# Optimization experiments

Hardware: AMD Instinct MI355X
Metric: run time of the kernel (lower is better)

## Reference

```python
import jax, jax.numpy as jnp
import numpy as np

B, N = 32, 64
ATTR, STATE, REL, GDIM = 4, 8, 4, 32
NF = 128

def _ln(x, w, b, eps=1e-5):
    mu = jnp.mean(x, axis=-1, keepdims=True)
    var = jnp.mean((x - mu) ** 2, axis=-1, keepdims=True)
    return (x - mu) * jax.lax.rsqrt(var + eps) * w + b

def setup_inputs() -> dict:
    key = jax.random.key(0)
    ks = iter(jax.random.split(key, 32))
    d = {}
    d['attrs'] = jax.random.normal(next(ks), (B, N, ATTR), jnp.float32)
    d['states'] = jax.random.normal(next(ks), (B, N, STATE), jnp.float32)
    d['actions'] = jnp.zeros((B, N, 4), jnp.float32)  # action=False, unused
    d['rel_attrs'] = jax.random.normal(next(ks), (B, N, N, REL), jnp.float32)
    def w(shape):
        return jax.random.normal(next(ks), shape, jnp.float32) * 0.05
    d['oe_w0'] = w((NF, ATTR + STATE)); d['oe_b0'] = jnp.zeros((NF,), jnp.float32)
    d['oe_w1'] = w((NF, NF));            d['oe_b1'] = jnp.zeros((NF,), jnp.float32)
    d['re_w0'] = w((NF, STATE + REL + 2 * ATTR)); d['re_b0'] = jnp.zeros((NF,), jnp.float32)
    d['re_w1'] = w((NF, NF));            d['re_b1'] = jnp.zeros((NF,), jnp.float32)
    d['rp_w'] = w((NF, NF + 2 * NF));    d['rp_b'] = jnp.zeros((NF,), jnp.float32)
    d['rp_lnw'] = jnp.ones((NF,), jnp.float32); d['rp_lnb'] = jnp.zeros((NF,), jnp.float32)
    d['pp_w'] = w((NF, 2 * NF));         d['pp_b'] = jnp.zeros((NF,), jnp.float32)
    d['pp_lnw'] = jnp.ones((NF,), jnp.float32); d['pp_lnb'] = jnp.zeros((NF,), jnp.float32)
    d['pr_w0'] = w((NF, NF));            d['pr_b0'] = jnp.zeros((NF,), jnp.float32)
    d['pr_w1'] = w((GDIM, NF));          d['pr_b1'] = jnp.zeros((GDIM,), jnp.float32)
    d['pstep'] = 2
    return d

def reference(attrs, states, actions, rel_attrs,
              oe_w0, oe_b0, oe_w1, oe_b1,
              re_w0, re_b0, re_w1, re_b1,
              rp_w, rp_b, rp_lnw, rp_lnb,
              pp_w, pp_b, pp_lnw, pp_lnb,
              pr_w0, pr_b0, pr_w1, pr_b1, pstep):
    lin = lambda x, w, b: jnp.einsum('...i,oi->...o', x, w) + b
    # ---- encode nodes: [B,N,attr+state] -> [B,N,NF] (action=False) ----
    obj_in = jnp.concatenate([attrs, states], axis=2)
    obj_encode = jax.nn.relu(lin(jax.nn.relu(lin(obj_in, oe_w0, oe_b0)), oe_w1, oe_b1))
    # ---- encode edges over dense N x N pairs ----
    rel_states = states[:, :, None, :] - states[:, None, :, :]        # B,N,N,state
    recv_attr = jnp.broadcast_to(attrs[:, :, None, :], (attrs.shape[0], attrs.shape[1], attrs.shape[1], attrs.shape[2]))
    send_attr = jnp.broadcast_to(attrs[:, None, :, :], recv_attr.shape)
    rel_in = jnp.concatenate([rel_attrs, rel_states, recv_attr, send_attr], axis=3)
    rel_encode = jax.nn.relu(lin(jax.nn.relu(lin(rel_in, re_w0, re_b0)), re_w1, re_b1))  # B,N,N,NF
    # ---- propagation steps ----
    for _ in range(pstep):
        sh = rel_encode.shape[:3] + (obj_encode.shape[-1],)
        recv = jnp.broadcast_to(obj_encode[:, :, None, :], sh)
        send = jnp.broadcast_to(obj_encode[:, None, :, :], sh)
        rel_effect = jax.nn.relu(_ln(lin(jnp.concatenate([rel_encode, recv, send], axis=3), rp_w, rp_b), rp_lnw, rp_lnb))
        rel_agg = rel_effect.sum(axis=2)                               # B,N,NF
        obj_encode = jax.nn.relu(_ln(lin(jnp.concatenate([obj_encode, rel_agg], axis=2), pp_w, pp_b), pp_lnw, pp_lnb))
    # ---- predict + tanh (state_encoder has tanh=True) ----
    out = lin(jax.nn.relu(lin(obj_encode, pr_w0, pr_b0)), pr_w1, pr_b1)
    return jnp.tanh(out)
```

## Files before the change

### kernel.cpp

```cpp
#include <hip/hip_runtime.h>
#include <hip/hip_bf16.h>


#define ROWS 2048
typedef unsigned short u16;
typedef unsigned int u32;
typedef __attribute__((ext_vector_type(8))) short bf16x8;
typedef __attribute__((ext_vector_type(4))) float f32x4;

__device__ __forceinline__ float bsu(u16 u) { return __uint_as_float(((u32)u) << 16); }
__device__ __forceinline__ u16 f2b(float f) {
    u32 u = __float_as_uint(f);
    u32 r = (u + 0x7fffu + ((u >> 16) & 1u)) >> 16;
    return (u16)r;
}
__device__ __forceinline__ u32 pk2(float a, float b) {
    __hip_bfloat162 h = __float22bfloat162_rn(float2{a, b});
    union { __hip_bfloat162 h; u32 u; } c; c.h = h; return c.u;
}
__device__ __forceinline__ bf16x8 ldcvt8(const float* __restrict__ p) {
    float4 a = *(const float4*)p;
    float4 b = *(const float4*)(p + 4);
    union { u32 u[4]; bf16x8 v; } x;
    x.u[0] = pk2(a.x, a.y); x.u[1] = pk2(a.z, a.w);
    x.u[2] = pk2(b.x, b.y); x.u[3] = pk2(b.z, b.w);
    return x.v;
}

__global__ __launch_bounds__(256)
void k_node(const float* __restrict__ attrs, const float* __restrict__ states,
            const float* __restrict__ oe_w0, const float* __restrict__ oe_b0,
            const float* __restrict__ oe_w1, const float* __restrict__ oe_b1,
            const float* __restrict__ re_w0, const float* __restrict__ re_b0,
            const float* __restrict__ rp_w,  const float* __restrict__ rp_b,
            const float* __restrict__ re_w1, const float* __restrict__ pp_w,
            const float* __restrict__ pr_w0, const float* __restrict__ pr_w1,
            u16* __restrict__ re_w1b, u16* __restrict__ web, u16* __restrict__ pp_wb,
            u16* __restrict__ wrecvb, u16* __restrict__ wsendb,
            u16* __restrict__ pr_w0b, u16* __restrict__ pr_w1b, u16* __restrict__ wsumb,
            u16* __restrict__ objb, float* __restrict__ nr, float* __restrict__ ns,
            float* __restrict__ recvT, float* __restrict__ sendT,
            float* __restrict__ recvS0, float* __restrict__ sendS0)
{
    const int r0 = blockIdx.x * 16;
    const int t = threadIdx.x;
    __shared__ float xs[16][12];
    __shared__ float w0s[1536];
    __shared__ float rw0s[2560];
    __shared__ __align__(16) u16 hb[16 * 136];
    __shared__ __align__(16) u16 ob[16 * 136];

    {
        int gid = blockIdx.x * 256 + t;
        for (int i = gid; i < 118784; i += 32768) {
            int idx = i;
            if (idx < 16384) { re_w1b[idx] = f2b(re_w1[idx]); continue; }
            idx -= 16384;
            if (idx < 16384) { web[idx] = f2b(rp_w[(idx >> 7) * 384 + (idx & 127)]); continue; }
            idx -= 16384;
            if (idx < 32768) { pp_wb[idx] = f2b(pp_w[idx]); continue; }
            idx -= 32768;
            if (idx < 16384) { wrecvb[idx] = f2b(rp_w[(idx >> 7) * 384 + 128 + (idx & 127)]); continue; }
            idx -= 16384;
            if (idx < 16384) { wsendb[idx] = f2b(rp_w[(idx >> 7) * 384 + 256 + (idx & 127)]); continue; }
            idx -= 16384;
            if (idx < 16384) { pr_w0b[idx] = f2b(pr_w0[idx]); continue; }
            idx -= 16384;
            pr_w1b[idx] = f2b(pr_w1[idx]);
        }
    }
    if (blockIdx.x == 0 && t < 128) {
        float s = 0.f;
        for (int o = 0; o < 128; o++) s += bsu(f2b(rp_w[o * 384 + t]));
        wsumb[t] = f2b(s);
    }

    if (t < 192) { int row = t / 12, c = t - row * 12;
        xs[row][c] = (c < 4) ? attrs[(r0 + row) * 4 + c] : states[(r0 + row) * 8 + (c - 4)]; }
    for (int i = t; i < 1536; i += 256) w0s[i] = oe_w0[i];
    for (int i = t; i < 2560; i += 256) rw0s[i] = re_w0[i];
    __syncthreads();

    for (int e = t; e < 2048; e += 256) {
        int row = e >> 7, o = e & 127;
        float h = oe_b0[o];
#pragma unroll
        for (int k = 0; k < 12; k++) h += w0s[o * 12 + k] * xs[row][k];
        hb[row * 136 + o] = f2b(fmaxf(h, 0.f));
        float s0 = 0.f, a0 = 0.f, a1 = 0.f;
#pragma unroll
        for (int k = 0; k < 8; k++) s0 += rw0s[o * 20 + 4 + k] * xs[row][4 + k];
#pragma unroll
        for (int k = 0; k < 4; k++) {
            a0 += rw0s[o * 20 + 12 + k] * xs[row][k];
            a1 += rw0s[o * 20 + 16 + k] * xs[row][k];
        }
        nr[(r0 + row) * 128 + o] = s0 + a0 + re_b0[o];
        ns[(r0 + row) * 128 + o] = a1 - s0;
    }
    __syncthreads();

    const int wave = t >> 6, lane = t & 63, tx = lane & 15, quad = lane >> 4;

    bf16x8 afr[4];
#pragma unroll
    for (int kk = 0; kk < 4; kk++) afr[kk] = *(const bf16x8*)&hb[tx * 136 + kk * 32 + quad * 8];
    f32x4 acc[2]; acc[0] = (f32x4){0.f,0.f,0.f,0.f}; acc[1] = acc[0];
#pragma unroll
    for (int ot = 0; ot < 2; ot++) {
        int o = (wave * 2 + ot) * 16 + tx;
#pragma unroll
        for (int kk = 0; kk < 4; kk++) {
            bf16x8 bfr = ldcvt8(&oe_w1[o * 128 + kk * 32 + quad * 8]);
            acc[ot] = __builtin_amdgcn_mfma_f32_16x16x32_bf16(afr[kk], bfr, acc[ot], 0, 0, 0);
        }
    }
#pragma unroll
    for (int ot = 0; ot < 2; ot++) {
        int o = (wave * 2 + ot) * 16 + tx;
        float bia = oe_b1[o];
#pragma unroll
        for (int r = 0; r < 4; r++)
            ob[(quad * 4 + r) * 136 + o] = f2b(fmaxf(acc[ot][r] + bia, 0.f));
    }
    __syncthreads();
    { int m = t >> 4, c = t & 15;
      *(uint4*)&objb[(r0 + m) * 128 + c * 8] = *(const uint4*)&ob[m * 136 + c * 8]; }

#pragma unroll
    for (int kk = 0; kk < 4; kk++) afr[kk] = *(const bf16x8*)&ob[tx * 136 + kk * 32 + quad * 8];
    f32x4 ar[2], an[2];
    ar[0] = (f32x4){0.f,0.f,0.f,0.f}; ar[1] = ar[0]; an[0] = ar[0]; an[1] = ar[0];
#pragma unroll
    for (int ot = 0; ot < 2; ot++) {
        int o = (wave * 2 + ot) * 16 + tx;
#pragma unroll
        for (int kk = 0; kk < 4; kk++) {
            bf16x8 br = ldcvt8(&rp_w[o * 384 + 128 + kk * 32 + quad * 8]);
            ar[ot] = __builtin_amdgcn_mfma_f32_16x16x32_bf16(afr[kk], br, ar[ot], 0, 0, 0);
            bf16x8 bs = ldcvt8(&rp_w[o * 384 + 256 + kk * 32 + quad * 8]);
            an[ot] = __builtin_amdgcn_mfma_f32_16x16x32_bf16(afr[kk], bs, an[ot], 0, 0, 0);
        }
    }
    float rbv[2] = { rp_b[(wave * 2 + 0) * 16 + tx], rp_b[(wave * 2 + 1) * 16 + tx] };
#pragma unroll
    for (int ot = 0; ot < 2; ot++) {
        int o = (wave * 2 + ot) * 16 + tx;
#pragma unroll
        for (int r = 0; r < 4; r++) {
            recvT[(r0 + quad * 4 + r) * 128 + o] = ar[ot][r] + rbv[ot];
            sendT[(r0 + quad * 4 + r) * 128 + o] = an[ot][r];
        }
    }
    __syncthreads();
    float* fr  = (float*)hb;
    float* fs2 = (float*)ob;
#pragma unroll
    for (int r = 0; r < 4; r++) {
        int row = quad * 4 + r;
        fr[row * 68 + wave * 16 + tx]  = (ar[0][r] + rbv[0]) + (ar[1][r] + rbv[1]);
        fs2[row * 68 + wave * 16 + tx] = an[0][r] + an[1][r];
    }
    __syncthreads();
    if (t < 32) {
        int p = t >> 4, row = t & 15;
        const float* src = p ? fs2 : fr;
        float s = 0.f;
#pragma unroll
        for (int k = 0; k < 64; k++) s += src[row * 68 + k];
        (p ? sendS0 : recvS0)[r0 + row] = s;
    }
}

__global__ __launch_bounds__(256)
void k_edge_fused(const float* __restrict__ rel_attrs,
                  const float* __restrict__ re_w0, const u16* __restrict__ re_w1b,
                  const u16* __restrict__ web, const u16* __restrict__ wsumb,
                  const float* __restrict__ re_b1,
                  const float* __restrict__ rp_lnw, const float* __restrict__ rp_lnb,
                  const float* __restrict__ nr, const float* __restrict__ ns,
                  const float* __restrict__ recvT, const float* __restrict__ sendT,
                  const float* __restrict__ recvS0, const float* __restrict__ sendS0,
                  u16* __restrict__ Ebuf, float* __restrict__ rowsumE,
                  u16* __restrict__ aggb)
{
    const int blkg = blockIdx.x;
    const int b = blkg >> 6;
    const int t = threadIdx.x;
    __shared__ __align__(16) u16 hsb[64 * 144];
    __shared__ float lnws[128], lnbs[128];
    __shared__ float redQ[256];

    if (t < 128) { lnws[t] = rp_lnw[t]; lnbs[t] = rp_lnb[t]; }

    {
        const int o0 = (t & 15) * 8;
        const int jb = t >> 4;
        float4 nr0 = *(const float4*)&nr[blkg * 128 + o0];
        float4 nr1 = *(const float4*)&nr[blkg * 128 + o0 + 4];
        float4 wreg[8];
#pragma unroll
        for (int k = 0; k < 8; k++) wreg[k] = *(const float4*)&re_w0[(o0 + k) * 20];
#pragma unroll
        for (int it = 0; it < 4; it++) {
            int j = jb + it * 16;
            float4 ra = *(const float4*)&rel_attrs[((size_t)blkg * 64 + j) * 4];
            const float* nsp = &ns[(b * 64 + j) * 128 + o0];
            float4 na = *(const float4*)nsp;
            float4 nb = *(const float4*)(nsp + 4);
            float v[8];
            v[0] = nr0.x + na.x; v[1] = nr0.y + na.y; v[2] = nr0.z + na.z; v[3] = nr0.w + na.w;
            v[4] = nr1.x + nb.x; v[5] = nr1.y + nb.y; v[6] = nr1.z + nb.z; v[7] = nr1.w + nb.w;
#pragma unroll
            for (int k = 0; k < 8; k++) {
                v[k] += wreg[k].x * ra.x + wreg[k].y * ra.y + wreg[k].z * ra.z + wreg[k].w * ra.w;
                v[k] = fmaxf(v[k], 0.f);
            }
            union { u32 u[4]; uint4 q; } p;
            p.u[0] = pk2(v[0], v[1]); p.u[1] = pk2(v[2], v[3]);
            p.u[2] = pk2(v[4], v[5]); p.u[3] = pk2(v[6], v[7]);
            *(uint4*)&hsb[j * 144 + o0] = p.q;
        }
    }

    const int w = t >> 6, lane = t & 63, tx = lane & 15, quad = lane >> 4;
    const int ob = w * 32;

    bf16x8 b1[2][4];
#pragma unroll
    for (int ot = 0; ot < 2; ot++)
#pragma unroll
        for (int kk = 0; kk < 4; kk++)
            b1[ot][kk] = *(const bf16x8*)&re_w1b[(ob + ot * 16 + tx) * 128 + kk * 32 + quad * 8];
    __syncthreads();

    f32x4 acc[4][2];
#pragma unroll
    for (int jt = 0; jt < 4; jt++) { acc[jt][0] = (f32x4){0.f,0.f,0.f,0.f}; acc[jt][1] = acc[jt][0]; }
#pragma unroll
    for (int jt = 0; jt < 4; jt++) {
        bf16x8 afr[4];
#pragma unroll
        for (int kk = 0; kk < 4; kk++)
            afr[kk] = *(const bf16x8*)&hsb[(jt * 16 + tx) * 144 + kk * 32 + quad * 8];
#pragma unroll
        for (int ot = 0; ot < 2; ot++)
#pragma unroll
            for (int kk = 0; kk < 4; kk++)
                acc[jt][ot] = __builtin_amdgcn_mfma_f32_16x16x32_bf16(afr[kk], b1[ot][kk], acc[jt][ot], 0, 0, 0);
    }
    __syncthreads();

    {
        float bia0 = re_b1[ob + tx], bia1 = re_b1[ob + 16 + tx];
#pragma unroll
        for (int jt = 0; jt < 4; jt++)
#pragma unroll
            for (int r = 0; r < 4; r++) {
                int j = jt * 16 + quad * 4 + r;
                hsb[j * 144 + ob + tx]      = f2b(fmaxf(acc[jt][0][r] + bia0, 0.f));
                hsb[j * 144 + ob + 16 + tx] = f2b(fmaxf(acc[jt][1][r] + bia1, 0.f));
            }
    }
    bf16x8 b2[2][4];
#pragma unroll
    for (int ot = 0; ot < 2; ot++)
#pragma unroll
        for (int kk = 0; kk < 4; kk++)
            b2[ot][kk] = *(const bf16x8*)&web[(ob + ot * 16 + tx) * 128 + kk * 32 + quad * 8];
    bf16x8 bws[4];
#pragma unroll
    for (int kk = 0; kk < 4; kk++)
        bws[kk] = *(const bf16x8*)&wsumb[kk * 32 + quad * 8];
    __syncthreads();

    f32x4 acc2[4][2], acc_ws[4];
#pragma unroll
    for (int jt = 0; jt < 4; jt++) {
        acc2[jt][0] = (f32x4){0.f,0.f,0.f,0.f}; acc2[jt][1] = acc2[jt][0];
        acc_ws[jt] = acc2[jt][0];
    }
#pragma unroll
    for (int jt = 0; jt < 4; jt++) {
        bf16x8 afr[4];
#pragma unroll
        for (int kk = 0; kk < 4; kk++)
            afr[kk] = *(const bf16x8*)&hsb[(jt * 16 + tx) * 144 + kk * 32 + quad * 8];
#pragma unroll
        for (int ot = 0; ot < 2; ot++)
#pragma unroll
            for (int kk = 0; kk < 4; kk++)
                acc2[jt][ot] = __builtin_amdgcn_mfma_f32_16x16x32_bf16(afr[kk], b2[ot][kk], acc2[jt][ot], 0, 0, 0);
#pragma unroll
        for (int kk = 0; kk < 4; kk++)
            acc_ws[jt] = __builtin_amdgcn_mfma_f32_16x16x32_bf16(afr[kk], bws[kk], acc_ws[jt], 0, 0, 0);
    }

#pragma unroll
    for (int jt = 0; jt < 4; jt++)
#pragma unroll
        for (int ot = 0; ot < 2; ot++) {
            uint2 ev;
            ev.x = pk2(acc2[jt][ot][0], acc2[jt][ot][1]);
            ev.y = pk2(acc2[jt][ot][2], acc2[jt][ot][3]);
            *(uint2*)(Ebuf + ((size_t)((blkg * 4 + jt) * 8 + (2 * w + ot)) * 64 + lane) * 4) = ev;
        }
    if (w == 0 && tx == 0) {
#pragma unroll
        for (int jt = 0; jt < 4; jt++)
            *(f32x4*)&rowsumE[(size_t)blkg * 64 + jt * 16 + quad * 4] = acc_ws[jt];
    }

    {
        float rv0 = recvT[blkg * 128 + ob + tx];
        float rv1 = recvT[blkg * 128 + ob + 16 + tx];
#pragma unroll
        for (int jt = 0; jt < 4; jt++)
#pragma unroll
            for (int r = 0; r < 4; r++) {
                int j = b * 64 + jt * 16 + quad * 4 + r;
                acc2[jt][0][r] += rv0 + sendT[j * 128 + ob + tx];
                acc2[jt][1][r] += rv1 + sendT[j * 128 + ob + 16 + tx];
            }
    }

#pragma unroll
    for (int jt = 0; jt < 4; jt++) {
        float q4[4];
#pragma unroll
        for (int r = 0; r < 4; r++) {
            float a0 = acc2[jt][0][r], a1 = acc2[jt][1][r];
            q4[r] = a0 * a0 + a1 * a1;
        }
#pragma unroll
        for (int m = 1; m < 16; m <<= 1)
#pragma unroll
            for (int r = 0; r < 4; r++) q4[r] += __shfl_xor(q4[r], m, 64);
        if (tx == 0)
#pragma unroll
            for (int r = 0; r < 4; r++) redQ[w * 64 + jt * 16 + quad * 4 + r] = q4[r];
    }
    __syncthreads();

    {
        float recvSi = recvS0[blkg];
        float lw0 = lnws[ob + tx], lb0 = lnbs[ob + tx];
        float lw1 = lnws[ob + 16 + tx], lb1 = lnbs[ob + 16 + tx];
        float ag0 = 0.f, ag1 = 0.f;
#pragma unroll
        for (int jt = 0; jt < 4; jt++) {
            f32x4 ssf = *(const f32x4*)&sendS0[b * 64 + jt * 16 + quad * 4];
#pragma unroll
            for (int r = 0; r < 4; r++) {
                int row = jt * 16 + quad * 4 + r;
                float qq = redQ[row] + redQ[64 + row] + redQ[128 + row] + redQ[192 + row];
                float mu = (acc_ws[jt][r] + recvSi + ssf[r]) * (1.f / 128.f);
                float rsd = rsqrtf(qq * (1.f / 128.f) - mu * mu + 1e-5f);
                float z0 = (acc2[jt][0][r] - mu) * rsd * lw0 + lb0;
                float z1 = (acc2[jt][1][r] - mu) * rsd * lw1 + lb1;
                ag0 += fmaxf(z0, 0.f);
                ag1 += fmaxf(z1, 0.f);
            }
        }
        ag0 += __shfl_xor(ag0, 16, 64); ag0 += __shfl_xor(ag0, 32, 64);
        ag1 += __shfl_xor(ag1, 16, 64); ag1 += __shfl_xor(ag1, 32, 64);
        if (quad == 0) {
            aggb[blkg * 128 + ob + tx]      = f2b(ag0);
            aggb[blkg * 128 + ob + 16 + tx] = f2b(ag1);
        }
    }
}

__global__ __launch_bounds__(256)
void k_prop_edge2(const u16* __restrict__ Ebuf, const float* __restrict__ rowsumE,
                  const float* __restrict__ rp_lnw, const float* __restrict__ rp_lnb,
                  const float* __restrict__ recvT, const float* __restrict__ sendT,
                  const float* __restrict__ recvS1, const float* __restrict__ sendS1,
                  u16* __restrict__ aggb)
{
    const int blk = blockIdx.x;
    const int b = blk >> 6;
    const int t = threadIdx.x;
    __shared__ float scr[16 * 132];
    __shared__ float lnws[128], lnbs[128];
    if (t < 128) { lnws[t] = rp_lnw[t]; lnbs[t] = rp_lnb[t]; }
    __syncthreads();

    const int wave = t >> 6, lane = t & 63, tx = lane & 15, quad = lane >> 4;
    const int tid = blk * 4 + wave;
    const int jrow = wave * 16 + quad * 4;

    float y[8][4];
#pragma unroll
    for (int oo = 0; oo < 8; oo++) {
        uint2 ev = *(const uint2*)(Ebuf + ((size_t)(tid * 8 + oo) * 64 + lane) * 4);
        const int o = oo * 16 + tx;
        float rv = recvT[blk * 128 + o];
        float e0 = bsu((u16)(ev.x & 0xffff)), e1 = bsu((u16)(ev.x >> 16));
        float e2 = bsu((u16)(ev.y & 0xffff)), e3 = bsu((u16)(ev.y >> 16));
        y[oo][0] = e0 + rv + sendT[(b * 64 + jrow + 0) * 128 + o];
        y[oo][1] = e1 + rv + sendT[(b * 64 + jrow + 1) * 128 + o];
        y[oo][2] = e2 + rv + sendT[(b * 64 + jrow + 2) * 128 + o];
        y[oo][3] = e3 + rv + sendT[(b * 64 + jrow + 3) * 128 + o];
    }
    float q[4];
#pragma unroll
    for (int r = 0; r < 4; r++) {
        q[r] = 0.f;
#pragma unroll
        for (int oo = 0; oo < 8; oo++) q[r] += y[oo][r] * y[oo][r];
    }
#pragma unroll
    for (int m = 1; m < 16; m <<= 1)
#pragma unroll
        for (int r = 0; r < 4; r++) q[r] += __shfl_xor(q[r], m, 64);

    float recvSi = recvS1[blk];
    f32x4 rse = *(const f32x4*)&rowsumE[(size_t)blk * 64 + jrow];
    f32x4 ssf = *(const f32x4*)&sendS1[b * 64 + jrow];
    float mu[4], rs[4];
#pragma unroll
    for (int r = 0; r < 4; r++) {
        mu[r] = (rse[r] + recvSi + ssf[r]) * (1.f / 128.f);
        rs[r] = rsqrtf(q[r] * (1.f / 128.f) - mu[r] * mu[r] + 1e-5f);
    }
    float pa[8];
#pragma unroll
    for (int oo = 0; oo < 8; oo++) {
        const int o = oo * 16 + tx;
        float lw = lnws[o], lb = lnbs[o];
        float p = 0.f;
#pragma unroll
        for (int r = 0; r < 4; r++) {
            float z = (y[oo][r] - mu[r]) * rs[r] * lw + lb;
            p += fmaxf(z, 0.f);
        }
        pa[oo] = p;
    }
    const int grp = wave * 4 + quad;
#pragma unroll
    for (int oo = 0; oo < 8; oo++) scr[grp * 132 + oo * 16 + tx] = pa[oo];
    __syncthreads();
    if (t < 128) {
        float sum = 0.f;
#pragma unroll
        for (int gg = 0; gg < 16; gg++) sum += scr[gg * 132 + t];
        aggb[blk * 128 + t] = f2b(sum);
    }
}

__global__ __launch_bounds__(256)
void k_pn0(const u16* __restrict__ aggb,
           const u16* __restrict__ pp_wb, const float* __restrict__ pp_b,
           const float* __restrict__ pp_lnw, const float* __restrict__ pp_lnb,
           const u16* __restrict__ wrecvb, const u16* __restrict__ wsendb,
           const float* __restrict__ rp_b,
           u16* __restrict__ objb, float* __restrict__ recvT, float* __restrict__ sendT,
           float* __restrict__ recvS1, float* __restrict__ sendS1)
{
    const int r0 = blockIdx.x * 16;
    const int t = threadIdx.x;
    __shared__ __align__(16) u16 ab[16 * 264];
    __shared__ __align__(16) u16 ob[16 * 136];
    __shared__ float redS[64], redQ[64];

    for (int i = t; i < 512; i += 256) {
        int m = i >> 5, c = i & 31;
        uint4 v = (c < 16) ? *(const uint4*)&objb[(r0 + m) * 128 + (c & 15) * 8]
                           : *(const uint4*)&aggb[(r0 + m) * 128 + (c - 16) * 8];
        *(uint4*)&ab[m * 264 + c * 8] = v;
    }
    __syncthreads();

    const int wave = t >> 6, lane = t & 63, tx = lane & 15, quad = lane >> 4;
    bf16x8 afr[8];
#pragma unroll
    for (int kk = 0; kk < 8; kk++) afr[kk] = *(const bf16x8*)&ab[tx * 264 + kk * 32 + quad * 8];
    f32x4 acc[2]; acc[0] = (f32x4){0.f,0.f,0.f,0.f}; acc[1] = acc[0];
#pragma unroll
    for (int ot = 0; ot < 2; ot++) {
        int o = (wave * 2 + ot) * 16 + tx;
#pragma unroll
        for (int kk = 0; kk < 8; kk++) {
            bf16x8 bfr = *(const bf16x8*)&pp_wb[o * 256 + kk * 32 + quad * 8];
            acc[ot] = __builtin_amdgcn_mfma_f32_16x16x32_bf16(afr[kk], bfr, acc[ot], 0, 0, 0);
        }
    }
#pragma unroll
    for (int ot = 0; ot < 2; ot++) {
        float bia = pp_b[(wave * 2 + ot) * 16 + tx];
#pragma unroll
        for (int r = 0; r < 4; r++) acc[ot][r] += bia;
    }

    float s[4], q[4];
#pragma unroll
    for (int r = 0; r < 4; r++) {
        s[r] = acc[0][r] + acc[1][r];
        q[r] = acc[0][r] * acc[0][r] + acc[1][r] * acc[1][r];
    }
#pragma unroll
    for (int m = 1; m < 16; m <<= 1) {
#pragma unroll
        for (int r = 0; r < 4; r++) {
            s[r] += __shfl_xor(s[r], m, 64);
            q[r] += __shfl_xor(q[r], m, 64);
        }
    }
    if (tx == 0) {
#pragma unroll
        for (int r = 0; r < 4; r++) {
            redS[wave * 16 + quad * 4 + r] = s[r];
            redQ[wave * 16 + quad * 4 + r] = q[r];
        }
    }
    __syncthreads();
    float mu[4], rs[4];
#pragma unroll
    for (int r = 0; r < 4; r++) {
        int m = quad * 4 + r;
        float ss = redS[m] + redS[16 + m] + redS[32 + m] + redS[48 + m];
        float qq = redQ[m] + redQ[16 + m] + redQ[32 + m] + redQ[48 + m];
        mu[r] = ss * (1.f / 128.f);
        rs[r] = rsqrtf(qq * (1.f / 128.f) - mu[r] * mu[r] + 1e-5f);
    }
#pragma unroll
    for (int ot = 0; ot < 2; ot++) {
        int o = (wave * 2 + ot) * 16 + tx;
        float lw = pp_lnw[o], lb = pp_lnb[o];
#pragma unroll
        for (int r = 0; r < 4; r++) {
            float z = (acc[ot][r] - mu[r]) * rs[r] * lw + lb;
            ob[(quad * 4 + r) * 136 + o] = f2b(fmaxf(z, 0.f));
        }
    }
    __syncthreads();
    { int m = t >> 4, c = t & 15;
      *(uint4*)&objb[(r0 + m) * 128 + c * 8] = *(const uint4*)&ob[m * 136 + c * 8]; }

    bf16x8 af2[4];
#pragma unroll
    for (int kk = 0; kk < 4; kk++) af2[kk] = *(const bf16x8*)&ob[tx * 136 + kk * 32 + quad * 8];
    f32x4 ar[2], an[2];
    ar[0] = (f32x4){0.f,0.f,0.f,0.f}; ar[1] = ar[0]; an[0] = ar[0]; an[1] = ar[0];
#pragma unroll
    for (int ot = 0; ot < 2; ot++) {
        int o = (wave * 2 + ot) * 16 + tx;
#pragma unroll
        for (int kk = 0; kk < 4; kk++) {
            bf16x8 br = *(const bf16x8*)&wrecvb[o * 128 + kk * 32 + quad * 8];
            ar[ot] = __builtin_amdgcn_mfma_f32_16x16x32_bf16(af2[kk], br, ar[ot], 0, 0, 0);
            bf16x8 bs = *(const bf16x8*)&wsendb[o * 128 + kk * 32 + quad * 8];
            an[ot] = __builtin_amdgcn_mfma_f32_16x16x32_bf16(af2[kk], bs, an[ot], 0, 0, 0);
        }
    }
    float rbv[2] = { rp_b[(wave * 2 + 0) * 16 + tx], rp_b[(wave * 2 + 1) * 16 + tx] };
#pragma unroll
    for (int ot = 0; ot < 2; ot++) {
        int o = (wave * 2 + ot) * 16 + tx;
#pragma unroll
        for (int r = 0; r < 4; r++) {
            recvT[(r0 + quad * 4 + r) * 128 + o] = ar[ot][r] + rbv[ot];
            sendT[(r0 + quad * 4 + r) * 128 + o] = an[ot][r];
        }
    }
    __syncthreads();
    float* fr  = (float*)ab;
    float* fs2 = ((float*)ab) + 1056;
#pragma unroll
    for (int r = 0; r < 4; r++) {
        int row = quad * 4 + r;
        fr[row * 66 + wave * 16 + tx]  = (ar[0][r] + rbv[0]) + (ar[1][r] + rbv[1]);
        fs2[row * 66 + wave * 16 + tx] = an[0][r] + an[1][r];
    }
    __syncthreads();
    if (t < 32) {
        int p = t >> 4, row = t & 15;
        const float* src = p ? fs2 : fr;
        float s2 = 0.f;
#pragma unroll
        for (int k = 0; k < 64; k++) s2 += src[row * 66 + k];
        (p ? sendS1 : recvS1)[r0 + row] = s2;
    }
}

__global__ __launch_bounds__(256)
void k_pn1pred(const u16* __restrict__ aggb,
               const u16* __restrict__ pp_wb, const float* __restrict__ pp_b,
               const float* __restrict__ pp_lnw, const float* __restrict__ pp_lnb,
               const u16* __restrict__ objb,
               const u16* __restrict__ pr_w0b, const float* __restrict__ pr_b0,
               const u16* __restrict__ pr_w1b, const float* __restrict__ pr_b1,
               float* __restrict__ out)
{
    const int r0 = blockIdx.x * 16;
    const int t = threadIdx.x;
    __shared__ __align__(16) u16 ab[16 * 264];
    __shared__ __align__(16) u16 ob[16 * 136];
    __shared__ __align__(16) u16 hb2[16 * 136];
    __shared__ float redS[64], redQ[64];

    for (int i = t; i < 512; i += 256) {
        int m = i >> 5, c = i & 31;
        uint4 v = (c < 16) ? *(const uint4*)&objb[(r0 + m) * 128 + (c & 15) * 8]
                           : *(const uint4*)&aggb[(r0 + m) * 128 + (c - 16) * 8];
        *(uint4*)&ab[m * 264 + c * 8] = v;
    }
    __syncthreads();

    const int wave = t >> 6, lane = t & 63, tx = lane & 15, quad = lane >> 4;
    bf16x8 afr[8];
#pragma unroll
    for (int kk = 0; kk < 8; kk++) afr[kk] = *(const bf16x8*)&ab[tx * 264 + kk * 32 + quad * 8];
    f32x4 acc[2]; acc[0] = (f32x4){0.f,0.f,0.f,0.f}; acc[1] = acc[0];
#pragma unroll
    for (int ot = 0; ot < 2; ot++) {
        int o = (wave * 2 + ot) * 16 + tx;
#pragma unroll
        for (int kk = 0; kk < 8; kk++) {
            bf16x8 bfr = *(const bf16x8*)&pp_wb[o * 256 + kk * 32 + quad * 8];
            acc[ot] = __builtin_amdgcn_mfma_f32_16x16x32_bf16(afr[kk], bfr, acc[ot], 0, 0, 0);
        }
    }
#pragma unroll
    for (int ot = 0; ot < 2; ot++) {
        float bia = pp_b[(wave * 2 + ot) * 16 + tx];
#pragma unroll
        for (int r = 0; r < 4; r++) acc[ot][r] += bia;
    }

    float s[4], q[4];
#pragma unroll
    for (int r = 0; r < 4; r++) {
        s[r] = acc[0][r] + acc[1][r];
        q[r] = acc[0][r] * acc[0][r] + acc[1][r] * acc[1][r];
    }
#pragma unroll
    for (int m = 1; m < 16; m <<= 1) {
#pragma unroll
        for (int r = 0; r < 4; r++) {
            s[r] += __shfl_xor(s[r], m, 64);
            q[r] += __shfl_xor(q[r], m, 64);
        }
    }
    if (tx == 0) {
#pragma unroll
        for (int r = 0; r < 4; r++) {
            redS[wave * 16 + quad * 4 + r] = s[r];
            redQ[wave * 16 + quad * 4 + r] = q[r];
        }
    }
    __syncthreads();
    float mu[4], rs[4];
#pragma unroll
    for (int r = 0; r < 4; r++) {
        int m = quad * 4 + r;
        float ss = redS[m] + redS[16 + m] + redS[32 + m] + redS[48 + m];
        float qq = redQ[m] + redQ[16 + m] + redQ[32 + m] + redQ[48 + m];
        mu[r] = ss * (1.f / 128.f);
        rs[r] = rsqrtf(qq * (1.f / 128.f) - mu[r] * mu[r] + 1e-5f);
    }
#pragma unroll
    for (int ot = 0; ot < 2; ot++) {
        int o = (wave * 2 + ot) * 16 + tx;
        float lw = pp_lnw[o], lb = pp_lnb[o];
#pragma unroll
        for (int r = 0; r < 4; r++) {
            float z = (acc[ot][r] - mu[r]) * rs[r] * lw + lb;
            ob[(quad * 4 + r) * 136 + o] = f2b(fmaxf(z, 0.f));
        }
    }
    __syncthreads();

    bf16x8 af2[4];
#pragma unroll
    for (int kk = 0; kk < 4; kk++) af2[kk] = *(const bf16x8*)&ob[tx * 136 + kk * 32 + quad * 8];
    f32x4 ah[2]; ah[0] = (f32x4){0.f,0.f,0.f,0.f}; ah[1] = ah[0];
#pragma unroll
    for (int ot = 0; ot < 2; ot++) {
        int o = (wave * 2 + ot) * 16 + tx;
#pragma unroll
        for (int kk = 0; kk < 4; kk++) {
            bf16x8 bfr = *(const bf16x8*)&pr_w0b[o * 128 + kk * 32 + quad * 8];
            ah[ot] = __builtin_amdgcn_mfma_f32_16x16x32_bf16(af2[kk], bfr, ah[ot], 0, 0, 0);
        }
    }
#pragma unroll
    for (int ot = 0; ot < 2; ot++) {
        int o = (wave * 2 + ot) * 16 + tx;
        float bia = pr_b0[o];
#pragma unroll
        for (int r = 0; r < 4; r++)
            hb2[(quad * 4 + r) * 136 + o] = f2b(fmaxf(ah[ot][r] + bia, 0.f));
    }
    __syncthreads();
    if (wave < 2) {
        bf16x8 af3[4];
#pragma unroll
        for (int kk = 0; kk < 4; kk++) af3[kk] = *(const bf16x8*)&hb2[tx * 136 + kk * 32 + quad * 8];
        f32x4 a2 = (f32x4){0.f,0.f,0.f,0.f};
        int o = wave * 16 + tx;
#pragma unroll
        for (int kk = 0; kk < 4; kk++) {
            bf16x8 bfr = *(const bf16x8*)&pr_w1b[o * 128 + kk * 32 + quad * 8];
            a2 = __builtin_amdgcn_mfma_f32_16x16x32_bf16(af3[kk], bfr, a2, 0, 0, 0);
        }
        float bia = pr_b1[o];
#pragma unroll
        for (int r = 0; r < 4; r++)
            out[(r0 + quad * 4 + r) * 32 + o] = tanhf(a2[r] + bia);
    }
}

extern "C" void kernel_launch(void* const* d_in, const int* in_sizes, int n_in,
                              void* d_out, int out_size, void* d_ws, size_t ws_size,
                              hipStream_t stream)
{
    const float* attrs    = (const float*)d_in[0];
    const float* states   = (const float*)d_in[1];
    const float* rel_attrs= (const float*)d_in[3];
    const float* oe_w0 = (const float*)d_in[4];
    const float* oe_b0 = (const float*)d_in[5];
    const float* oe_w1 = (const float*)d_in[6];
    const float* oe_b1 = (const float*)d_in[7];
    const float* re_w0 = (const float*)d_in[8];
    const float* re_b0 = (const float*)d_in[9];
    const float* re_w1 = (const float*)d_in[10];
    const float* re_b1 = (const float*)d_in[11];
    const float* rp_w  = (const float*)d_in[12];
    const float* rp_b  = (const float*)d_in[13];
    const float* rp_lnw= (const float*)d_in[14];
    const float* rp_lnb= (const float*)d_in[15];
    const float* pp_w  = (const float*)d_in[16];
    const float* pp_b  = (const float*)d_in[17];
    const float* pp_lnw= (const float*)d_in[18];
    const float* pp_lnb= (const float*)d_in[19];
    const float* pr_w0 = (const float*)d_in[20];
    const float* pr_b0 = (const float*)d_in[21];
    const float* pr_w1 = (const float*)d_in[22];
    const float* pr_b1 = (const float*)d_in[23];

    float* ws     = (float*)d_ws;
    float* nr     = ws;
    float* ns     = nr    + ROWS * 128;
    float* recvT  = ns    + ROWS * 128;
    float* sendT  = recvT + ROWS * 128;
    float* recvS0 = sendT + ROWS * 128;
    float* sendS0 = recvS0 + ROWS;
    float* recvS1 = sendS0 + ROWS;
    float* sendS1 = recvS1 + ROWS;
    float* rowsumE= sendS1 + ROWS;
    u16* wsumb  = (u16*)(rowsumE + ROWS * 64);
    u16* re_w1b = wsumb + 128;
    u16* web    = re_w1b + 16384;
    u16* pp_wb  = web    + 16384;
    u16* wrecvb = pp_wb  + 32768;
    u16* wsendb = wrecvb + 16384;
    u16* pr_w0b = wsendb + 16384;
    u16* pr_w1b = pr_w0b + 16384;
    u16* objb   = pr_w1b + 4096;
    u16* aggb   = objb + ROWS * 128;
    u16* Ebuf   = aggb + ROWS * 128;

    k_node<<<128, 256, 0, stream>>>(attrs, states, oe_w0, oe_b0, oe_w1, oe_b1,
                                    re_w0, re_b0, rp_w, rp_b,
                                    re_w1, pp_w, pr_w0, pr_w1,
                                    re_w1b, web, pp_wb, wrecvb, wsendb, pr_w0b, pr_w1b, wsumb,
                                    objb, nr, ns, recvT, sendT, recvS0, sendS0);
    k_edge_fused<<<2048, 256, 0, stream>>>(rel_attrs, re_w0, re_w1b, web, wsumb, re_b1,
                                           rp_lnw, rp_lnb, nr, ns, recvT, sendT,
                                           recvS0, sendS0, Ebuf, rowsumE, aggb);
    k_pn0<<<128, 256, 0, stream>>>(aggb, pp_wb, pp_b, pp_lnw, pp_lnb,
                                   wrecvb, wsendb, rp_b, objb, recvT, sendT,
                                   recvS1, sendS1);
    k_prop_edge2<<<2048, 256, 0, stream>>>(Ebuf, rowsumE, rp_lnw, rp_lnb,
                                           recvT, sendT, recvS1, sendS1, aggb);
    k_pn1pred<<<128, 256, 0, stream>>>(aggb, pp_wb, pp_b, pp_lnw, pp_lnb, objb,
                                       pr_w0b, pr_b0, pr_w1b, pr_b1, (float*)d_out);
}
```

Before: 191.1 us.

## Fuse node-update and prediction MLPs into per-row edge kernel epilogues

Removes the two small node kernels, k_pn0 and k_pn1pred. Their work (node LayerNorm update, recv/send projections, and the final predictor MLP with tanh) moves into the tails of the two 2048-block edge kernels, one block per node row. It uses scalar dot products against newly transposed bf16 weights so that loads coalesce across output columns. The goal is to save launch overhead and the aggb round trip through global memory. The cost is that every block re-reads the full weight matrices from L2 and does the matvecs in scalar FMA instead of MFMA.

```diff
diff --git a/kernel.cpp b/kernel.cpp
--- a/kernel.cpp
+++ b/kernel.cpp
@@ -35,9 +35,9 @@
             const float* __restrict__ rp_w,  const float* __restrict__ rp_b,
             const float* __restrict__ re_w1, const float* __restrict__ pp_w,
             const float* __restrict__ pr_w0, const float* __restrict__ pr_w1,
-            u16* __restrict__ re_w1b, u16* __restrict__ web, u16* __restrict__ pp_wb,
-            u16* __restrict__ wrecvb, u16* __restrict__ wsendb,
-            u16* __restrict__ pr_w0b, u16* __restrict__ pr_w1b, u16* __restrict__ wsumb,
+            u16* __restrict__ re_w1b, u16* __restrict__ web, u16* __restrict__ pp_wT,
+            u16* __restrict__ wrecvT, u16* __restrict__ wsendT,
+            u16* __restrict__ pr_w0T, u16* __restrict__ pr_w1T, u16* __restrict__ wsumb,
             u16* __restrict__ objb, float* __restrict__ nr, float* __restrict__ ns,
             float* __restrict__ recvT, float* __restrict__ sendT,
             float* __restrict__ recvS0, float* __restrict__ sendS0)
@@ -58,15 +58,19 @@
             idx -= 16384;
             if (idx < 16384) { web[idx] = f2b(rp_w[(idx >> 7) * 384 + (idx & 127)]); continue; }
             idx -= 16384;
-            if (idx < 32768) { pp_wb[idx] = f2b(pp_w[idx]); continue; }
+            if (idx < 32768) { int k = idx >> 7, o = idx & 127;
+                pp_wT[idx] = f2b(pp_w[o * 256 + k]); continue; }
             idx -= 32768;
-            if (idx < 16384) { wrecvb[idx] = f2b(rp_w[(idx >> 7) * 384 + 128 + (idx & 127)]); continue; }
+            if (idx < 16384) { int k = idx >> 7, o = idx & 127;
+                wrecvT[idx] = f2b(rp_w[o * 384 + 128 + k]); continue; }
             idx -= 16384;
-            if (idx < 16384) { wsendb[idx] = f2b(rp_w[(idx >> 7) * 384 + 256 + (idx & 127)]); continue; }
+            if (idx < 16384) { int k = idx >> 7, o = idx & 127;
+                wsendT[idx] = f2b(rp_w[o * 384 + 256 + k]); continue; }
             idx -= 16384;
-            if (idx < 16384) { pr_w0b[idx] = f2b(pr_w0[idx]); continue; }
+            if (idx < 16384) { int k = idx >> 7, o = idx & 127;
+                pr_w0T[idx] = f2b(pr_w0[o * 128 + k]); continue; }
             idx -= 16384;
-            pr_w1b[idx] = f2b(pr_w1[idx]);
+            { int k = idx >> 5, o = idx & 31; pr_w1T[idx] = f2b(pr_w1[o * 128 + k]); }
         }
     }
     if (blockIdx.x == 0 && t < 128) {
@@ -181,8 +185,15 @@
                   const float* __restrict__ nr, const float* __restrict__ ns,
                   const float* __restrict__ recvT, const float* __restrict__ sendT,
                   const float* __restrict__ recvS0, const float* __restrict__ sendS0,
+                  const u16* __restrict__ objb,
+                  const u16* __restrict__ pp_wT, const float* __restrict__ pp_b,
+                  const float* __restrict__ pp_lnw, const float* __restrict__ pp_lnb,
+                  const u16* __restrict__ wrecvT, const u16* __restrict__ wsendT,
+                  const float* __restrict__ rp_b,
                   u16* __restrict__ Ebuf, float* __restrict__ rowsumE,
-                  u16* __restrict__ aggb)
+                  u16* __restrict__ obj1b, float* __restrict__ recvT1,
+                  float* __restrict__ sendT1,
+                  float* __restrict__ recvS1v, float* __restrict__ sendS1v)
 {
     const int blkg = blockIdx.x;
     const int b = blkg >> 6;
@@ -190,6 +201,9 @@
     __shared__ __align__(16) u16 hsb[64 * 144];
     __shared__ float lnws[128], lnbs[128];
     __shared__ float redQ[256];
+    __shared__ float xv[256];
+    __shared__ float part[256];
+    __shared__ float red2[8];
 
     if (t < 128) { lnws[t] = rp_lnw[t]; lnbs[t] = rp_lnb[t]; }
 
@@ -365,24 +379,81 @@
         ag0 += __shfl_xor(ag0, 16, 64); ag0 += __shfl_xor(ag0, 32, 64);
         ag1 += __shfl_xor(ag1, 16, 64); ag1 += __shfl_xor(ag1, 32, 64);
         if (quad == 0) {
-            aggb[blkg * 128 + ob + tx]      = f2b(ag0);
-            aggb[blkg * 128 + ob + 16 + tx] = f2b(ag1);
-        }
-    }
+            xv[128 + ob + tx]      = ag0;
+            xv[128 + ob + 16 + tx] = ag1;
+        }
+    }
+    if (t < 128) xv[t] = bsu(objb[blkg * 128 + t]);
+    __syncthreads();
+
+    {
+        int o = t & 127, h = t >> 7;
+        const u16* wp = pp_wT + h * 128 * 128 + o;
+        const float* xp = xv + h * 128;
+        float p = 0.f;
+#pragma unroll 16
+        for (int kk = 0; kk < 128; kk++) p += xp[kk] * bsu(wp[kk * 128]);
+        part[t] = p;
+    }
+    __syncthreads();
+    float val = 0.f;
+    if (t < 128) {
+        val = part[t] + part[128 + t] + pp_b[t];
+        float s = val, q = val * val;
+#pragma unroll
+        for (int m = 1; m < 64; m <<= 1) { s += __shfl_xor(s, m, 64); q += __shfl_xor(q, m, 64); }
+        if (lane == 0) { red2[w * 2] = s; red2[w * 2 + 1] = q; }
+    }
+    __syncthreads();
+    if (t < 128) {
+        float ss = red2[0] + red2[2], qq = red2[1] + red2[3];
+        float mu = ss * (1.f / 128.f);
+        float rsd = rsqrtf(qq * (1.f / 128.f) - mu * mu + 1e-5f);
+        float z = (val - mu) * rsd * pp_lnw[t] + pp_lnb[t];
+        float o1 = fmaxf(z, 0.f);
+        obj1b[blkg * 128 + t] = f2b(o1);
+        xv[t] = o1;
+    }
+    __syncthreads();
+    {
+        int o = t & 127;
+        const u16* wT = (t < 128) ? wrecvT : wsendT;
+        float a = 0.f;
+#pragma unroll 16
+        for (int k = 0; k < 128; k++) a += xv[k] * bsu(wT[k * 128 + o]);
+        if (t < 128) a += rp_b[o];
+        float s = a;
+#pragma unroll
+        for (int m = 1; m < 64; m <<= 1) s += __shfl_xor(s, m, 64);
+        if (lane == 0) red2[4 + w] = s;
+        if (t < 128) recvT1[blkg * 128 + o] = a;
+        else         sendT1[blkg * 128 + o] = a;
+    }
+    __syncthreads();
+    if (t == 0) recvS1v[blkg] = red2[4] + red2[5];
+    else if (t == 128) sendS1v[blkg] = red2[6] + red2[7];
 }
 
 __global__ __launch_bounds__(256)
 void k_prop_edge2(const u16* __restrict__ Ebuf, const float* __restrict__ rowsumE,
                   const float* __restrict__ rp_lnw, const float* __restrict__ rp_lnb,
-                  const float* __restrict__ recvT, const float* __restrict__ sendT,
-                  const float* __restrict__ recvS1, const float* __restrict__ sendS1,
-                  u16* __restrict__ aggb)
+                  const float* __restrict__ recvT1, const float* __restrict__ sendT1,
+                  const float* __restrict__ recvS1v, const float* __restrict__ sendS1v,
+                  const u16* __restrict__ obj1b,
+                  const u16* __restrict__ pp_wT, const float* __restrict__ pp_b,
+                  const float* __restrict__ pp_lnw, const float* __restrict__ pp_lnb,
+                  const u16* __restrict__ pr_w0T, const float* __restrict__ pr_b0,
+                  const u16* __restrict__ pr_w1T, const float* __restrict__ pr_b1,
+                  float* __restrict__ out)
 {
     const int blk = blockIdx.x;
     const int b = blk >> 6;
     const int t = threadIdx.x;
     __shared__ float scr[16 * 132];
     __shared__ float lnws[128], lnbs[128];
+    __shared__ float xv[256];
+    __shared__ float part[256];
+    __shared__ float red2[8];
     if (t < 128) { lnws[t] = rp_lnw[t]; lnbs[t] = rp_lnb[t]; }
     __syncthreads();
 
@@ -395,13 +466,13 @@
     for (int oo = 0; oo < 8; oo++) {
         uint2 ev = *(const uint2*)(Ebuf + ((size_t)(tid * 8 + oo) * 64 + lane) * 4);
         const int o = oo * 16 + tx;
-        float rv = recvT[blk * 128 + o];
+        float rv = recvT1[blk * 128 + o];
         float e0 = bsu((u16)(ev.x & 0xffff)), e1 = bsu((u16)(ev.x >> 16));
         float e2 = bsu((u16)(ev.y & 0xffff)), e3 = bsu((u16)(ev.y >> 16));
-        y[oo][0] = e0 + rv + sendT[(b * 64 + jrow + 0) * 128 + o];
-        y[oo][1] = e1 + rv + sendT[(b * 64 + jrow + 1) * 128 + o];
-        y[oo][2] = e2 + rv + sendT[(b * 64 + jrow + 2) * 128 + o];
-        y[oo][3] = e3 + rv + sendT[(b * 64 + jrow + 3) * 128 + o];
+        y[oo][0] = e0 + rv + sendT1[(b * 64 + jrow + 0) * 128 + o];
+        y[oo][1] = e1 + rv + sendT1[(b * 64 + jrow + 1) * 128 + o];
+        y[oo][2] = e2 + rv + sendT1[(b * 64 + jrow + 2) * 128 + o];
+        y[oo][3] = e3 + rv + sendT1[(b * 64 + jrow + 3) * 128 + o];
     }
     float q[4];
 #pragma unroll
@@ -415,9 +486,9 @@
 #pragma unroll
         for (int r = 0; r < 4; r++) q[r] += __shfl_xor(q[r], m, 64);
 
-    float recvSi = recvS1[blk];
+    float recvSi = recvS1v[blk];
     f32x4 rse = *(const f32x4*)&rowsumE[(size_t)blk * 64 + jrow];
-    f32x4 ssf = *(const f32x4*)&sendS1[b * 64 + jrow];
+    f32x4 ssf = *(const f32x4*)&sendS1v[b * 64 + jrow];
     float mu[4], rs[4];
 #pragma unroll
     for (int r = 0; r < 4; r++) {
@@ -440,275 +511,73 @@
     const int grp = wave * 4 + quad;
 #pragma unroll
     for (int oo = 0; oo < 8; oo++) scr[grp * 132 + oo * 16 + tx] = pa[oo];
+    if (t < 128) xv[t] = bsu(obj1b[blk * 128 + t]);
     __syncthreads();
     if (t < 128) {
         float sum = 0.f;
 #pragma unroll
         for (int gg = 0; gg < 16; gg++) sum += scr[gg * 132 + t];
-        aggb[blk * 128 + t] = f2b(sum);
-    }
-}
-
-__global__ __launch_bounds__(256)
-void k_pn0(const u16* __restrict__ aggb,
-           const u16* __restrict__ pp_wb, const float* __restrict__ pp_b,
-           const float* __restrict__ pp_lnw, const float* __restrict__ pp_lnb,
-           const u16* __restrict__ wrecvb, const u16* __restrict__ wsendb,
-           const float* __restrict__ rp_b,
-           u16* __restrict__ objb, float* __restrict__ recvT, float* __restrict__ sendT,
-           float* __restrict__ recvS1, float* __restrict__ sendS1)
-{
-    const int r0 = blockIdx.x * 16;
-    const int t = threadIdx.x;
-    __shared__ __align__(16) u16 ab[16 * 264];
-    __shared__ __align__(16) u16 ob[16 * 136];
-    __shared__ float redS[64], redQ[64];
-
-    for (int i = t; i < 512; i += 256) {
-        int m = i >> 5, c = i & 31;
-        uint4 v = (c < 16) ? *(const uint4*)&objb[(r0 + m) * 128 + (c & 15) * 8]
-                           : *(const uint4*)&aggb[(r0 + m) * 128 + (c - 16) * 8];
-        *(uint4*)&ab[m * 264 + c * 8] = v;
-    }
-    __syncthreads();
-
-    const int wave = t >> 6, lane = t & 63, tx = lane & 15, quad = lane >> 4;
-    bf16x8 afr[8];
-#pragma unroll
-    for (int kk = 0; kk < 8; kk++) afr[kk] = *(const bf16x8*)&ab[tx * 264 + kk * 32 + quad * 8];
-    f32x4 acc[2]; acc[0] = (f32x4){0.f,0.f,0.f,0.f}; acc[1] = acc[0];
-#pragma unroll
-    for (int ot = 0; ot < 2; ot++) {
-        int o = (wave * 2 + ot) * 16 + tx;
-#pragma unroll
-        for (int kk = 0; kk < 8; kk++) {
-            bf16x8 bfr = *(const bf16x8*)&pp_wb[o * 256 + kk * 32 + quad * 8];
-            acc[ot] = __builtin_amdgcn_mfma_f32_16x16x32_bf16(afr[kk], bfr, acc[ot], 0, 0, 0);
-        }
-    }
-#pragma unroll
-    for (int ot = 0; ot < 2; ot++) {
-        float bia = pp_b[(wave * 2 + ot) * 16 + tx];
-#pragma unroll
-        for (int r = 0; r < 4; r++) acc[ot][r] += bia;
-    }
-
-    float s[4], q[4];
-#pragma unroll
-    for (int r = 0; r < 4; r++) {
-        s[r] = acc[0][r] + acc[1][r];
-        q[r] = acc[0][r] * acc[0][r] + acc[1][r] * acc[1][r];
-    }
-#pragma unroll
-    for (int m = 1; m < 16; m <<= 1) {
-#pragma unroll
-        for (int r = 0; r < 4; r++) {
-            s[r] += __shfl_xor(s[r], m, 64);
-            q[r] += __shfl_xor(q[r], m, 64);
-        }
-    }
-    if (tx == 0) {
-#pragma unroll
-        for (int r = 0; r < 4; r++) {
-            redS[wave * 16 + quad * 4 + r] = s[r];
-            redQ[wave * 16 + quad * 4 + r] = q[r];
-        }
-    }
-    __syncthreads();
-    float mu[4], rs[4];
-#pragma unroll
-    for (int r = 0; r < 4; r++) {
-        int m = quad * 4 + r;
-        float ss = redS[m] + redS[16 + m] + redS[32 + m] + redS[48 + m];
-        float qq = redQ[m] + redQ[16 + m] + redQ[32 + m] + redQ[48 + m];
-        mu[r] = ss * (1.f / 128.f);
-        rs[r] = rsqrtf(qq * (1.f / 128.f) - mu[r] * mu[r] + 1e-5f);
-    }
-#pragma unroll
-    for (int ot = 0; ot < 2; ot++) {
-        int o = (wave * 2 + ot) * 16 + tx;
-        float lw = pp_lnw[o], lb = pp_lnb[o];
-#pragma unroll
-        for (int r = 0; r < 4; r++) {
-            float z = (acc[ot][r] - mu[r]) * rs[r] * lw + lb;
-            ob[(quad * 4 + r) * 136 + o] = f2b(fmaxf(z, 0.f));
-        }
-    }
-    __syncthreads();
-    { int m = t >> 4, c = t & 15;
-      *(uint4*)&objb[(r0 + m) * 128 + c * 8] = *(const uint4*)&ob[m * 136 + c * 8]; }
-
-    bf16x8 af2[4];
-#pragma unroll
-    for (int kk = 0; kk < 4; kk++) af2[kk] = *(const bf16x8*)&ob[tx * 136 + kk * 32 + quad * 8];
-    f32x4 ar[2], an[2];
-    ar[0] = (f32x4){0.f,0.f,0.f,0.f}; ar[1] = ar[0]; an[0] = ar[0]; an[1] = ar[0];
-#pragma unroll
-    for (int ot = 0; ot < 2; ot++) {
-        int o = (wave * 2 + ot) * 16 + tx;
-#pragma unroll
-        for (int kk = 0; kk < 4; kk++) {
-            bf16x8 br = *(const bf16x8*)&wrecvb[o * 128 + kk * 32 + quad * 8];
-            ar[ot] = __builtin_amdgcn_mfma_f32_16x16x32_bf16(af2[kk], br, ar[ot], 0, 0, 0);
-            bf16x8 bs = *(const bf16x8*)&wsendb[o * 128 + kk * 32 + quad * 8];
-            an[ot] = __builtin_amdgcn_mfma_f32_16x16x32_bf16(af2[kk], bs, an[ot], 0, 0, 0);
-        }
-    }
-    float rbv[2] = { rp_b[(wave * 2 + 0) * 16 + tx], rp_b[(wave * 2 + 1) * 16 + tx] };
-#pragma unroll
-    for (int ot = 0; ot < 2; ot++) {
-        int o = (wave * 2 + ot) * 16 + tx;
-#pragma unroll
-        for (int r = 0; r < 4; r++) {
-            recvT[(r0 + quad * 4 + r) * 128 + o] = ar[ot][r] + rbv[ot];
-            sendT[(r0 + quad * 4 + r) * 128 + o] = an[ot][r];
-        }
-    }
-    __syncthreads();
-    float* fr  = (float*)ab;
-    float* fs2 = ((float*)ab) + 1056;
-#pragma unroll
-    for (int r = 0; r < 4; r++) {
-        int row = quad * 4 + r;
-        fr[row * 66 + wave * 16 + tx]  = (ar[0][r] + rbv[0]) + (ar[1][r] + rbv[1]);
-        fs2[row * 66 + wave * 16 + tx] = an[0][r] + an[1][r];
+        xv[128 + t] = sum;
+    }
+    __syncthreads();
+
+    {
+        int o = t & 127, h = t >> 7;
+        const u16* wp = pp_wT + h * 128 * 128 + o;
+        const float* xp = xv + h * 128;
+        float p = 0.f;
+#pragma unroll 16
+        for (int kk = 0; kk < 128; kk++) p += xp[kk] * bsu(wp[kk * 128]);
+        part[t] = p;
+    }
+    __syncthreads();
+    float val = 0.f;
+    if (t < 128) {
+        val = part[t] + part[128 + t] + pp_b[t];
+        float s = val, qq2 = val * val;
+#pragma unroll
+        for (int m = 1; m < 64; m <<= 1) { s += __shfl_xor(s, m, 64); qq2 += __shfl_xor(qq2, m, 64); }
+        if (lane == 0) { red2[wave * 2] = s; red2[wave * 2 + 1] = qq2; }
+    }
+    __syncthreads();
+    if (t < 128) {
+        float ss = red2[0] + red2[2], qq = red2[1] + red2[3];
+        float muv = ss * (1.f / 128.f);
+        float rsd = rsqrtf(qq * (1.f / 128.f) - muv * muv + 1e-5f);
+        float z = (val - muv) * rsd * pp_lnw[t] + pp_lnb[t];
+        xv[t] = fmaxf(z, 0.f);
+    }
+    __syncthreads();
+
+    {
+        int o = t & 127, h = t >> 7;
+        const u16* wp = pr_w0T + h * 64 * 128 + o;
+        const float* xp = xv + h * 64;
+        float p = 0.f;
+#pragma unroll 16
+        for (int kk = 0; kk < 64; kk++) p += xp[kk] * bsu(wp[kk * 128]);
+        part[t] = p;
+    }
+    __syncthreads();
+    if (t < 128) {
+        float hv = fmaxf(part[t] + part[128 + t] + pr_b0[t], 0.f);
+        xv[128 + t] = hv;
+    }
+    __syncthreads();
+
+    if (t < 128) {
+        int o = t & 31, kq = t >> 5;
+        const u16* wp = pr_w1T + kq * 32 * 32 + o;
+        const float* hp = xv + 128 + kq * 32;
+        float p = 0.f;
+#pragma unroll
+        for (int kk = 0; kk < 32; kk++) p += hp[kk] * bsu(wp[kk * 32]);
+        part[t] = p;
     }
     __syncthreads();
     if (t < 32) {
-        int p = t >> 4, row = t & 15;
-        const float* src = p ? fs2 : fr;
-        float s2 = 0.f;
-#pragma unroll
-        for (int k = 0; k < 64; k++) s2 += src[row * 66 + k];
-        (p ? sendS1 : recvS1)[r0 + row] = s2;
-    }
-}
-
-__global__ __launch_bounds__(256)
-void k_pn1pred(const u16* __restrict__ aggb,
-               const u16* __restrict__ pp_wb, const float* __restrict__ pp_b,
-               const float* __restrict__ pp_lnw, const float* __restrict__ pp_lnb,
-               const u16* __restrict__ objb,
-               const u16* __restrict__ pr_w0b, const float* __restrict__ pr_b0,
-               const u16* __restrict__ pr_w1b, const float* __restrict__ pr_b1,
-               float* __restrict__ out)
-{
-    const int r0 = blockIdx.x * 16;
-    const int t = threadIdx.x;
-    __shared__ __align__(16) u16 ab[16 * 264];
-    __shared__ __align__(16) u16 ob[16 * 136];
-    __shared__ __align__(16) u16 hb2[16 * 136];
-    __shared__ float redS[64], redQ[64];
-
-    for (int i = t; i < 512; i += 256) {
-        int m = i >> 5, c = i & 31;
-        uint4 v = (c < 16) ? *(const uint4*)&objb[(r0 + m) * 128 + (c & 15) * 8]
-                           : *(const uint4*)&aggb[(r0 + m) * 128 + (c - 16) * 8];
-        *(uint4*)&ab[m * 264 + c * 8] = v;
-    }
-    __syncthreads();
-
-    const int wave = t >> 6, lane = t & 63, tx = lane & 15, quad = lane >> 4;
-    bf16x8 afr[8];
-#pragma unroll
-    for (int kk = 0; kk < 8; kk++) afr[kk] = *(const bf16x8*)&ab[tx * 264 + kk * 32 + quad * 8];
-    f32x4 acc[2]; acc[0] = (f32x4){0.f,0.f,0.f,0.f}; acc[1] = acc[0];
-#pragma unroll
-    for (int ot = 0; ot < 2; ot++) {
-        int o = (wave * 2 + ot) * 16 + tx;
-#pragma unroll
-        for (int kk = 0; kk < 8; kk++) {
-            bf16x8 bfr = *(const bf16x8*)&pp_wb[o * 256 + kk * 32 + quad * 8];
-            acc[ot] = __builtin_amdgcn_mfma_f32_16x16x32_bf16(afr[kk], bfr, acc[ot], 0, 0, 0);
-        }
-    }
-#pragma unroll
-    for (int ot = 0; ot < 2; ot++) {
-        float bia = pp_b[(wave * 2 + ot) * 16 + tx];
-#pragma unroll
-        for (int r = 0; r < 4; r++) acc[ot][r] += bia;
-    }
-
-    float s[4], q[4];
-#pragma unroll
-    for (int r = 0; r < 4; r++) {
-        s[r] = acc[0][r] + acc[1][r];
-        q[r] = acc[0][r] * acc[0][r] + acc[1][r] * acc[1][r];
-    }
-#pragma unroll
-    for (int m = 1; m < 16; m <<= 1) {
-#pragma unroll
-        for (int r = 0; r < 4; r++) {
-            s[r] += __shfl_xor(s[r], m, 64);
-            q[r] += __shfl_xor(q[r], m, 64);
-        }
-    }
-    if (tx == 0) {
-#pragma unroll
-        for (int r = 0; r < 4; r++) {
-            redS[wave * 16 + quad * 4 + r] = s[r];
-            redQ[wave * 16 + quad * 4 + r] = q[r];
-        }
-    }
-    __syncthreads();
-    float mu[4], rs[4];
-#pragma unroll
-    for (int r = 0; r < 4; r++) {
-        int m = quad * 4 + r;
-        float ss = redS[m] + redS[16 + m] + redS[32 + m] + redS[48 + m];
-        float qq = redQ[m] + redQ[16 + m] + redQ[32 + m] + redQ[48 + m];
-        mu[r] = ss * (1.f / 128.f);
-        rs[r] = rsqrtf(qq * (1.f / 128.f) - mu[r] * mu[r] + 1e-5f);
-    }
-#pragma unroll
-    for (int ot = 0; ot < 2; ot++) {
-        int o = (wave * 2 + ot) * 16 + tx;
-        float lw = pp_lnw[o], lb = pp_lnb[o];
-#pragma unroll
-        for (int r = 0; r < 4; r++) {
-            float z = (acc[ot][r] - mu[r]) * rs[r] * lw + lb;
-            ob[(quad * 4 + r) * 136 + o] = f2b(fmaxf(z, 0.f));
-        }
-    }
-    __syncthreads();
-
-    bf16x8 af2[4];
-#pragma unroll
-    for (int kk = 0; kk < 4; kk++) af2[kk] = *(const bf16x8*)&ob[tx * 136 + kk * 32 + quad * 8];
-    f32x4 ah[2]; ah[0] = (f32x4){0.f,0.f,0.f,0.f}; ah[1] = ah[0];
-#pragma unroll
-    for (int ot = 0; ot < 2; ot++) {
-        int o = (wave * 2 + ot) * 16 + tx;
-#pragma unroll
-        for (int kk = 0; kk < 4; kk++) {
-            bf16x8 bfr = *(const bf16x8*)&pr_w0b[o * 128 + kk * 32 + quad * 8];
-            ah[ot] = __builtin_amdgcn_mfma_f32_16x16x32_bf16(af2[kk], bfr, ah[ot], 0, 0, 0);
-        }
-    }
-#pragma unroll
-    for (int ot = 0; ot < 2; ot++) {
-        int o = (wave * 2 + ot) * 16 + tx;
-        float bia = pr_b0[o];
-#pragma unroll
-        for (int r = 0; r < 4; r++)
-            hb2[(quad * 4 + r) * 136 + o] = f2b(fmaxf(ah[ot][r] + bia, 0.f));
-    }
-    __syncthreads();
-    if (wave < 2) {
-        bf16x8 af3[4];
-#pragma unroll
-        for (int kk = 0; kk < 4; kk++) af3[kk] = *(const bf16x8*)&hb2[tx * 136 + kk * 32 + quad * 8];
-        f32x4 a2 = (f32x4){0.f,0.f,0.f,0.f};
-        int o = wave * 16 + tx;
-#pragma unroll
-        for (int kk = 0; kk < 4; kk++) {
-            bf16x8 bfr = *(const bf16x8*)&pr_w1b[o * 128 + kk * 32 + quad * 8];
-            a2 = __builtin_amdgcn_mfma_f32_16x16x32_bf16(af3[kk], bfr, a2, 0, 0, 0);
-        }
-        float bia = pr_b1[o];
-#pragma unroll
-        for (int r = 0; r < 4; r++)
-            out[(r0 + quad * 4 + r) * 32 + o] = tanhf(a2[r] + bia);
+        float a = part[t] + part[32 + t] + part[64 + t] + part[96 + t] + pr_b1[t];
+        out[blk * 32 + t] = tanhf(a);
     }
 }
 
@@ -740,41 +609,44 @@
     const float* pr_w1 = (const float*)d_in[22];
     const float* pr_b1 = (const float*)d_in[23];
 
-    float* ws     = (float*)d_ws;
-    float* nr     = ws;
-    float* ns     = nr    + ROWS * 128;
-    float* recvT  = ns    + ROWS * 128;
-    float* sendT  = recvT + ROWS * 128;
-    float* recvS0 = sendT + ROWS * 128;
-    float* sendS0 = recvS0 + ROWS;
-    float* recvS1 = sendS0 + ROWS;
-    float* sendS1 = recvS1 + ROWS;
-    float* rowsumE= sendS1 + ROWS;
+    float* ws      = (float*)d_ws;
+    float* nr      = ws;
+    float* ns      = nr + ROWS * 128;
+    float* recvT   = ns + ROWS * 128;
+    float* sendT   = recvT + ROWS * 128;
+    float* recvT1  = sendT + ROWS * 128;
+    float* sendT1  = recvT1 + ROWS * 128;
+    float* recvS0  = sendT1 + ROWS * 128;
+    float* sendS0  = recvS0 + ROWS;
+    float* recvS1v = sendS0 + ROWS;
+    float* sendS1v = recvS1v + ROWS;
+    float* rowsumE = sendS1v + ROWS;
     u16* wsumb  = (u16*)(rowsumE + ROWS * 64);
     u16* re_w1b = wsumb + 128;
     u16* web    = re_w1b + 16384;
-    u16* pp_wb  = web    + 16384;
-    u16* wrecvb = pp_wb  + 32768;
-    u16* wsendb = wrecvb + 16384;
-    u16* pr_w0b = wsendb + 16384;
-    u16* pr_w1b = pr_w0b + 16384;
-    u16* objb   = pr_w1b + 4096;
-    u16* aggb   = objb + ROWS * 128;
-    u16* Ebuf   = aggb + ROWS * 128;
+    u16* pp_wT  = web + 16384;
+    u16* wrecvT = pp_wT + 32768;
+    u16* wsendT = wrecvT + 16384;
+    u16* pr_w0T = wsendT + 16384;
+    u16* pr_w1T = pr_w0T + 16384;
+    u16* objb   = pr_w1T + 4096;
+    u16* obj1b  = objb + ROWS * 128;
+    u16* Ebuf   = obj1b + ROWS * 128;
 
     k_node<<<128, 256, 0, stream>>>(attrs, states, oe_w0, oe_b0, oe_w1, oe_b1,
                                     re_w0, re_b0, rp_w, rp_b,
                                     re_w1, pp_w, pr_w0, pr_w1,
-                                    re_w1b, web, pp_wb, wrecvb, wsendb, pr_w0b, pr_w1b, wsumb,
+                                    re_w1b, web, pp_wT, wrecvT, wsendT, pr_w0T, pr_w1T, wsumb,
                                     objb, nr, ns, recvT, sendT, recvS0, sendS0);
     k_edge_fused<<<2048, 256, 0, stream>>>(rel_attrs, re_w0, re_w1b, web, wsumb, re_b1,
                                            rp_lnw, rp_lnb, nr, ns, recvT, sendT,
-                                           recvS0, sendS0, Ebuf, rowsumE, aggb);
-    k_pn0<<<128, 256, 0, stream>>>(aggb, pp_wb, pp_b, pp_lnw, pp_lnb,
-                                   wrecvb, wsendb, rp_b, objb, recvT, sendT,
-                                   recvS1, sendS1);
+                                           recvS0, sendS0, objb,
+                                           pp_wT, pp_b, pp_lnw, pp_lnb,
+                                           wrecvT, wsendT, rp_b,
+                                           Ebuf, rowsumE, obj1b, recvT1, sendT1,
+                                           recvS1v, sendS1v);
     k_prop_edge2<<<2048, 256, 0, stream>>>(Ebuf, rowsumE, rp_lnw, rp_lnb,
-                                           recvT, sendT, recvS1, sendS1, aggb);
-    k_pn1pred<<<128, 256, 0, stream>>>(aggb, pp_wb, pp_b, pp_lnw, pp_lnb, objb,
-                                       pr_w0b, pr_b0, pr_w1b, pr_b1, (float*)d_out);
+                                           recvT1, sendT1, recvS1v, sendS1v,
+                                           obj1b, pp_wT, pp_b, pp_lnw, pp_lnb,
+                                           pr_w0T, pr_b0, pr_w1T, pr_b1, (float*)d_out);
 }
```

After: 208.5 us. 9.1% more time.
